# Kernel tuning notes

Measured on AMD Instinct MI355X. Metric: run time of the kernel, lower is better.

## Reference

```python
import jax, jax.numpy as jnp
import numpy as np
import math

B, S, H = 2, 2048, 2048
NH, NKV, HD = 16, 4, 128


def _rope_tables(seq_len, head_dim):
    # Standard RoPE: freqs over half dim, duplicated to full head_dim.
    inv_freq = 1.0 / (10000.0 ** (np.arange(0, head_dim, 2, dtype=np.float32) / head_dim))
    t = np.arange(seq_len, dtype=np.float32)
    freqs = np.outer(t, inv_freq)  # [S, HD/2]
    emb = np.concatenate([freqs, freqs], axis=-1)  # [S, HD]
    return jnp.asarray(np.cos(emb)), jnp.asarray(np.sin(emb))


def setup_inputs() -> dict:
    key = jax.random.key(0)
    k1, k2, k3, k4 = jax.random.split(key, 4)
    cos, sin = _rope_tables(S, HD)
    return {
        "x": jax.random.normal(k1, (B, S, H), dtype=jnp.float32),
        "cos": cos,
        "sin": sin,
        "Wq": jax.random.normal(k2, (H, NH * HD), dtype=jnp.float32) * (1.0 / math.sqrt(H)),
        "Wkv": jax.random.normal(k3, (H, 2 * NKV * HD), dtype=jnp.float32) * (1.0 / math.sqrt(H)),
        "Wo": jax.random.normal(k4, (NH * HD, H), dtype=jnp.float32) * (1.0 / math.sqrt(NH * HD)),
    }


def _rotate_half(x):
    x1, x2 = jnp.split(x, 2, axis=-1)
    return jnp.concatenate([-x2, x1], axis=-1)


def _apply_rotary(x, cos, sin):
    # x: [B, S, nheads, HD]; cos/sin: [S, HD]
    c = cos[None, :, None, :]
    s = sin[None, :, None, :]
    return x * c + _rotate_half(x) * s


def reference(x, cos, sin, Wq, Wkv, Wo):
    b, s, _ = x.shape
    q = (x @ Wq).reshape(b, s, NH, HD)
    kv = x @ Wkv
    k, v = jnp.split(kv, [NKV * HD], axis=-1)
    k = k.reshape(b, s, NKV, HD)
    v = v.reshape(b, s, NKV, HD)
    q = _apply_rotary(q, cos, sin)
    k = _apply_rotary(k, cos, sin)
    # to [B, heads, S, HD]
    q = jnp.transpose(q, (0, 2, 1, 3))
    k = jnp.transpose(k, (0, 2, 1, 3))
    v = jnp.transpose(v, (0, 2, 1, 3))
    # GQA: repeat K/V heads
    rep = NH // NKV
    k = jnp.repeat(k, rep, axis=1)
    v = jnp.repeat(v, rep, axis=1)
    scale = jnp.asarray(1.0 / math.sqrt(HD), dtype=x.dtype)
    scores = jnp.einsum('bhqd,bhkd->bhqk', q * scale, k)  # [B, NH, S, S]
    causal = jnp.tril(jnp.ones((s, s), dtype=jnp.bool_))
    scores = jnp.where(causal, scores, jnp.asarray(-jnp.inf, scores.dtype))
    attn = jax.nn.softmax(scores, axis=-1)
    out = jnp.einsum('bhqk,bhkd->bhqd', attn, v)
    out = jnp.transpose(out, (0, 2, 1, 3)).reshape(b, s, NH * HD)
    return out @ Wo
```

## Files before the change

kernel.cpp:

```cpp
#include <hip/hip_runtime.h>
#include <math.h>

#define NB 2
#define SEQ 2048
#define HDIM 2048
#define NHD 16
#define NKVH 4
#define HEADD 128
#define MROWS (NB*SEQ)
#define NQCOLS (NHD*HEADD)
#define QKVCOLS 3072

typedef unsigned short ushortT;
typedef __attribute__((ext_vector_type(8))) short short8;
typedef __attribute__((ext_vector_type(4))) float floatx4;
typedef __attribute__((ext_vector_type(4))) unsigned short ushort4v;

__device__ __forceinline__ ushortT f2bf(float f) {
  union { float f; unsigned int u; } v; v.f = f;
  unsigned int r = v.u + 0x7FFFu + ((v.u >> 16) & 1u);
  return (ushortT)(r >> 16);
}
__device__ __forceinline__ float bf2f(ushortT u) {
  union { unsigned int u; float f; } v; v.u = ((unsigned int)u) << 16;
  return v.f;
}

__device__ __forceinline__ unsigned int cvt_pk_bf16(float lo, float hi) {
  unsigned int r;
  asm("v_cvt_pk_bf16_f32 %0, %1, %2" : "=v"(r) : "v"(lo), "v"(hi));
  return r;
}

__device__ __forceinline__ void gload16(const ushortT* g, ushortT* l) {
  __builtin_amdgcn_global_load_lds(
      (const __attribute__((address_space(1))) void*)g,
      (__attribute__((address_space(3))) void*)l, 16, 0, 0);
}

__global__ __launch_bounds__(256) void cast_bf16_kernel(
    const float* __restrict__ in, ushortT* __restrict__ out, int n4) {
  int i = blockIdx.x * 256 + threadIdx.x;
  if (i >= n4) return;
  float4 v = ((const float4*)in)[i];
  ushort4v o;
  o.x = f2bf(v.x); o.y = f2bf(v.y); o.z = f2bf(v.z); o.w = f2bf(v.w);
  ((ushort4v*)out)[i] = o;
}

__global__ __launch_bounds__(256) void transpose_cast_kernel(
    const float* __restrict__ in, ushortT* __restrict__ out, int R, int C) {
  __shared__ ushortT tile[32][33];
  int c0 = blockIdx.x * 32, r0 = blockIdx.y * 32;
  int tx = threadIdx.x & 31, ty = threadIdx.x >> 5;
#pragma unroll
  for (int i = 0; i < 4; ++i)
    tile[ty + i*8][tx] = f2bf(in[(size_t)(r0 + ty + i*8) * C + c0 + tx]);
  __syncthreads();
#pragma unroll
  for (int i = 0; i < 4; ++i)
    out[(size_t)(c0 + ty + i*8) * R + r0 + tx] = tile[tx][ty + i*8];
}

__global__ __launch_bounds__(256) void gemm_bt_kernel(
    const ushortT* __restrict__ A, const ushortT* __restrict__ Bt,
    void* __restrict__ C, int M, int N, int K, int c_fp32) {
  __shared__ __align__(16) ushortT lA[128 * 64];
  __shared__ __align__(16) ushortT lB[128 * 64];
  const int m0 = blockIdx.y * 128;
  const int n0 = blockIdx.x * 128;
  const int tid = threadIdx.x;
  const int wave = tid >> 6, lane = tid & 63;
  const int g = lane >> 4, l15 = lane & 15;
  const int wm = (wave >> 1) * 64, wn = (wave & 1) * 64;
  const int sw = l15 & 7;

  floatx4 acc[4][4] = {};

  for (int kt = 0; kt < K; kt += 64) {
    __syncthreads();
#pragma unroll
    for (int i = 0; i < 4; ++i) {
      int s = i * 256 + tid;
      int r = s >> 3, j = s & 7;
      int col8 = j ^ (r & 7);
      gload16(A  + (size_t)(m0 + r) * K + kt + col8 * 8, lA + s * 8);
      gload16(Bt + (size_t)(n0 + r) * K + kt + col8 * 8, lB + s * 8);
    }
    __syncthreads();
#pragma unroll
    for (int ks = 0; ks < 2; ++ks) {
      short8 af[4], bfv[4];
#pragma unroll
      for (int t = 0; t < 4; ++t) {
        af[t]  = *(const short8*)(lA + (wm + t * 16 + l15) * 64 + ((ks * 4 + g) ^ sw) * 8);
        bfv[t] = *(const short8*)(lB + (wn + t * 16 + l15) * 64 + ((ks * 4 + g) ^ sw) * 8);
      }
#pragma unroll
      for (int mt = 0; mt < 4; ++mt)
#pragma unroll
        for (int nt = 0; nt < 4; ++nt)
          acc[mt][nt] = __builtin_amdgcn_mfma_f32_16x16x32_bf16(
              af[mt], bfv[nt], acc[mt][nt], 0, 0, 0);
    }
  }

#pragma unroll
  for (int mt = 0; mt < 4; ++mt)
#pragma unroll
    for (int nt = 0; nt < 4; ++nt)
#pragma unroll
      for (int r = 0; r < 4; ++r) {
        int row = m0 + wm + mt * 16 + g * 4 + r;
        int col = n0 + wn + nt * 16 + l15;
        float v = acc[mt][nt][r];
        if (c_fp32) ((float*)C)[(size_t)row * N + col] = v;
        else ((ushortT*)C)[(size_t)row * N + col] = f2bf(v);
      }
}

__global__ __launch_bounds__(256) void rope_q_kernel(
    const ushortT* __restrict__ QKVtmp, const float* __restrict__ cosT,
    const float* __restrict__ sinT, ushortT* __restrict__ Qr) {
  int idx = blockIdx.x * 256 + threadIdx.x;
  int d = idx & 63;
  int t = idx >> 6;
  int h = t & (NHD - 1);
  int bs = t >> 4;
  int s = bs & (SEQ - 1);
  int b = bs >> 11;
  float c = cosT[s * HEADD + d], sn = sinT[s * HEADD + d];
  float q1 = bf2f(QKVtmp[(size_t)bs * QKVCOLS + h * HEADD + d]);
  float q2 = bf2f(QKVtmp[(size_t)bs * QKVCOLS + h * HEADD + d + 64]);
  size_t o = ((size_t)(b * NHD + h) * SEQ + s) * HEADD + d;
  Qr[o]      = f2bf(q1 * c - q2 * sn);
  Qr[o + 64] = f2bf(q2 * c + q1 * sn);
}

__global__ __launch_bounds__(256) void rope_k_kernel(
    const ushortT* __restrict__ QKVtmp, const float* __restrict__ cosT,
    const float* __restrict__ sinT, ushortT* __restrict__ Kr) {
  int idx = blockIdx.x * 256 + threadIdx.x;
  int d = idx & 63;
  int t = idx >> 6;
  int kvh = t & (NKVH - 1);
  int bs = t >> 2;
  int s = bs & (SEQ - 1);
  int b = bs >> 11;
  float c = cosT[s * HEADD + d], sn = sinT[s * HEADD + d];
  float k1 = bf2f(QKVtmp[(size_t)bs * QKVCOLS + 2048 + kvh * HEADD + d]);
  float k2 = bf2f(QKVtmp[(size_t)bs * QKVCOLS + 2048 + kvh * HEADD + d + 64]);
  size_t o = ((size_t)(b * NKVH + kvh) * SEQ + s) * HEADD + d;
  Kr[o]      = f2bf(k1 * c - k2 * sn);
  Kr[o + 64] = f2bf(k2 * c + k1 * sn);
}

__global__ __launch_bounds__(256) void v_relayout_kernel(
    const ushortT* __restrict__ QKVtmp, ushortT* __restrict__ Vt) {
  __shared__ ushortT tile[32][33];
  int bk = blockIdx.z;
  int b = bk >> 2, kvh = bk & 3;
  int s0 = blockIdx.x * 32, d0 = blockIdx.y * 32;
  int tx = threadIdx.x & 31, ty = threadIdx.x >> 5;
#pragma unroll
  for (int i = 0; i < 4; ++i) {
    int s = s0 + ty + i * 8;
    tile[ty + i * 8][tx] =
        QKVtmp[(size_t)(b * SEQ + s) * QKVCOLS + 2560 + kvh * HEADD + d0 + tx];
  }
  __syncthreads();
#pragma unroll
  for (int i = 0; i < 4; ++i) {
    int d = d0 + ty + i * 8;
    Vt[((size_t)bk * HEADD + d) * SEQ + s0 + tx] = tile[tx][ty + i * 8];
  }
}

__global__ __launch_bounds__(256) void attn_kernel(
    const ushortT* __restrict__ Q,
    const ushortT* __restrict__ Kg,
    const ushortT* __restrict__ Vg,
    ushortT* __restrict__ Oa) {
  __shared__ __align__(16) ushortT lK[64 * 128];
  __shared__ __align__(16) ushortT lV[128 * 64];
  __shared__ __align__(16) ushortT lP[4 * 16 * 64];

  const int tid = threadIdx.x;
  const int w = tid >> 6, lane = tid & 63;
  const int g = lane >> 4, l15 = lane & 15;
  const int sw = l15 & 7;
  const int bh = blockIdx.x;
  const int b = bh >> 4, h = bh & 15;
  const int kvh = h >> 2;
  const int qi = 31 - (int)blockIdx.y;
  const int q0 = qi << 6;
  const int qw = q0 + w * 16;

  const float SC = 0.08838834764831845f * 1.4426950408889634f;
  const float THR = 8.0f / SC;

  short8 qf[4];
  {
    const ushortT* qp =
        Q + (((size_t)(b * NHD + h)) * SEQ + qw + l15) * HEADD + g * 8;
#pragma unroll
    for (int ks = 0; ks < 4; ++ks) qf[ks] = *(const short8*)(qp + ks * 32);
  }

  floatx4 o[8] = {};
  float m_s = -INFINITY;
  float l_s = 0.f;

  const ushortT* kbase = Kg + ((size_t)(b * NKVH + kvh)) * SEQ * HEADD;
  const ushortT* vbase = Vg + ((size_t)(b * NKVH + kvh)) * HEADD * SEQ;
  ushortT* pw = lP + w * 16 * 64;

  const int nkt = qi + 1;
  for (int kt = 0; kt < nkt; ++kt) {
    __syncthreads();
#pragma unroll
    for (int ii = 0; ii < 4; ++ii) {
      int s = ii * 256 + tid;
      int r = s >> 4, j = (s & 15) ^ (r & 7);
      gload16(kbase + (size_t)(kt * 64 + r) * HEADD + j * 8, lK + s * 8);
    }
#pragma unroll
    for (int ii = 0; ii < 4; ++ii) {
      int s = ii * 256 + tid;
      int r = s >> 3, j = (s & 7) ^ (r & 7);
      gload16(vbase + (size_t)r * SEQ + kt * 64 + j * 8, lV + s * 8);
    }
    __syncthreads();

    const int rel = qw - kt * 64;

    floatx4 sc[4] = {};
    __builtin_amdgcn_s_setprio(1);
#pragma unroll
    for (int nt = 0; nt < 4; ++nt) {
      if (nt * 16 > rel + 15) continue;
#pragma unroll
      for (int ks = 0; ks < 4; ++ks) {
        short8 kf = *(const short8*)(lK + (nt * 16 + l15) * 128 + ((ks * 4 + g) ^ sw) * 8);
        sc[nt] = __builtin_amdgcn_mfma_f32_16x16x32_bf16(kf, qf[ks], sc[nt], 0, 0, 0);
      }
    }
    __builtin_amdgcn_s_setprio(0);

    const bool needmask = (kt * 64 + 63) > qw;
    float ps[4][4];
    float mx = -INFINITY;
#pragma unroll
    for (int nt = 0; nt < 4; ++nt)
#pragma unroll
      for (int r = 0; r < 4; ++r) {
        float v = sc[nt][r];
        if (needmask) {
          int kg = kt * 64 + nt * 16 + g * 4 + r;
          if (kg > qw + l15) v = -INFINITY;
        }
        ps[nt][r] = v;
        mx = fmaxf(mx, v);
      }
    mx = fmaxf(mx, __shfl_xor(mx, 16));
    mx = fmaxf(mx, __shfl_xor(mx, 32));

    float mn;
    if (__all(mx <= m_s + THR)) {
      mn = m_s;
    } else {
      mn = fmaxf(m_s, mx);
      float alpha = __builtin_amdgcn_exp2f((m_s - mn) * SC);
      l_s *= alpha;
#pragma unroll
      for (int dt = 0; dt < 8; ++dt)
#pragma unroll
        for (int r = 0; r < 4; ++r) o[dt][r] *= alpha;
      m_s = mn;
    }
    const float mnSC = mn * SC;

    float rs = 0.f;
#pragma unroll
    for (int nt = 0; nt < 4; ++nt) {
      float e[4];
#pragma unroll
      for (int r = 0; r < 4; ++r) {
        e[r] = __builtin_amdgcn_exp2f(__builtin_fmaf(ps[nt][r], SC, -mnSC));
        rs += e[r];
      }
      uint2 pk;
      pk.x = cvt_pk_bf16(e[0], e[1]);
      pk.y = cvt_pk_bf16(e[2], e[3]);
      *(uint2*)(pw + l15 * 64 + (((nt * 2 + (g >> 1)) ^ sw) * 8 + (g & 1) * 4)) = pk;
    }
    rs += __shfl_xor(rs, 16);
    rs += __shfl_xor(rs, 32);
    l_s += rs;

    __builtin_amdgcn_s_setprio(1);
#pragma unroll
    for (int ks = 0; ks < 2; ++ks) {
      if (kt * 64 + ks * 32 > qw + 15) continue;
      short8 bp = *(const short8*)(pw + l15 * 64 + ((ks * 4 + g) ^ sw) * 8);
#pragma unroll
      for (int dt = 0; dt < 8; ++dt) {
        short8 vf = *(const short8*)(lV + (dt * 16 + l15) * 64 + ((ks * 4 + g) ^ sw) * 8);
        o[dt] = __builtin_amdgcn_mfma_f32_16x16x32_bf16(vf, bp, o[dt], 0, 0, 0);
      }
    }
    __builtin_amdgcn_s_setprio(0);
  }

  {
    float inv = 1.f / l_s;
    int qg = qw + l15;
#pragma unroll
    for (int dt = 0; dt < 8; ++dt) {
      uint2 ov;
      ov.x = cvt_pk_bf16(o[dt][0] * inv, o[dt][1] * inv);
      ov.y = cvt_pk_bf16(o[dt][2] * inv, o[dt][3] * inv);
      *(uint2*)(Oa + (size_t)(b * SEQ + qg) * NQCOLS + h * HEADD + dt * 16 + g * 4) = ov;
    }
  }
}

extern "C" void kernel_launch(void* const* d_in, const int* in_sizes, int n_in,
                              void* d_out, int out_size, void* d_ws, size_t ws_size,
                              hipStream_t stream) {
  const float* x    = (const float*)d_in[0];
  const float* cosT = (const float*)d_in[1];
  const float* sinT = (const float*)d_in[2];
  const float* Wq   = (const float*)d_in[3];
  const float* Wkv  = (const float*)d_in[4];
  const float* Wo   = (const float*)d_in[5];

  char* ws = (char*)d_ws;
  ushortT* x_bf   = (ushortT*)(ws + 0);
  ushortT* Wqkvt  = (ushortT*)(ws + 16777216);
  ushortT* Wot    = (ushortT*)(ws + 29360128);
  ushortT* QKVtmp = (ushortT*)(ws + 37748736);
  ushortT* Qr     = (ushortT*)(ws + 62914560);
  ushortT* Kr     = (ushortT*)(ws + 79691776);
  ushortT* Vt     = (ushortT*)(ws + 83886080);
  ushortT* Oattn  = QKVtmp;

  cast_bf16_kernel<<<8192, 256, 0, stream>>>(x, x_bf, (MROWS * HDIM) / 4);
  transpose_cast_kernel<<<dim3(64, 64), 256, 0, stream>>>(Wq, Wqkvt, HDIM, NQCOLS);
  transpose_cast_kernel<<<dim3(32, 64), 256, 0, stream>>>(Wkv, Wqkvt + 2048 * 2048, HDIM, 1024);
  transpose_cast_kernel<<<dim3(64, 64), 256, 0, stream>>>(Wo, Wot, NQCOLS, HDIM);

  gemm_bt_kernel<<<dim3(24, 32), 256, 0, stream>>>(x_bf, Wqkvt, QKVtmp, MROWS, QKVCOLS, HDIM, 0);

  rope_q_kernel<<<16384, 256, 0, stream>>>(QKVtmp, cosT, sinT, Qr);
  rope_k_kernel<<<4096, 256, 0, stream>>>(QKVtmp, cosT, sinT, Kr);
  v_relayout_kernel<<<dim3(64, 4, 8), 256, 0, stream>>>(QKVtmp, Vt);

  attn_kernel<<<dim3(32, 32), 256, 0, stream>>>(Qr, Kr, Vt, Oattn);

  gemm_bt_kernel<<<dim3(16, 32), 256, 0, stream>>>(Oattn, Wot, d_out, MROWS, HDIM, NQCOLS, 1);
}
```

Baseline: 339.2 us.

## Pair causal query tiles per block and double-buffer K/V loads

Each attention block now processes two query tiles, one long and one short in causal length (qi=31-y and qi=y). This evens out the work per block and halves the grid. K/V tiles are double-buffered in LDS, so the next tile's global-to-LDS load is issued before the current tile's compute, with one barrier per iteration. The cost is twice the K/V LDS footprint, which may reduce occupancy, and more registers for the two Q fragment sets.

```diff
diff --git a/kernel.cpp b/kernel.cpp
--- a/kernel.cpp
+++ b/kernel.cpp
@@ -181,8 +181,8 @@
     const ushortT* __restrict__ Kg,
     const ushortT* __restrict__ Vg,
     ushortT* __restrict__ Oa) {
-  __shared__ __align__(16) ushortT lK[64 * 128];
-  __shared__ __align__(16) ushortT lV[128 * 64];
+  __shared__ __align__(16) ushortT lK[2][64 * 128];
+  __shared__ __align__(16) ushortT lV[2][128 * 64];
   __shared__ __align__(16) ushortT lP[4 * 16 * 64];
 
   const int tid = threadIdx.x;
@@ -192,57 +192,63 @@
   const int bh = blockIdx.x;
   const int b = bh >> 4, h = bh & 15;
   const int kvh = h >> 2;
-  const int qi = 31 - (int)blockIdx.y;
-  const int q0 = qi << 6;
-  const int qw = q0 + w * 16;
+  const int yi = blockIdx.y;
+  const int qiA = 31 - yi;
+  const int qiB = yi;
+  const int nA = qiA + 1, nB = qiB + 1;
 
   const float SC = 0.08838834764831845f * 1.4426950408889634f;
   const float THR = 8.0f / SC;
 
-  short8 qf[4];
+  const ushortT* kbase = Kg + ((size_t)(b * NKVH + kvh)) * SEQ * HEADD;
+  const ushortT* vbase = Vg + ((size_t)(b * NKVH + kvh)) * HEADD * SEQ;
+  ushortT* pw = lP + w * 16 * 64;
+
+  const int qwA = (qiA << 6) + w * 16;
+  const int qwB = (qiB << 6) + w * 16;
+
+  short8 qfA[4], qfB[4];
   {
-    const ushortT* qp =
-        Q + (((size_t)(b * NHD + h)) * SEQ + qw + l15) * HEADD + g * 8;
-#pragma unroll
-    for (int ks = 0; ks < 4; ++ks) qf[ks] = *(const short8*)(qp + ks * 32);
+    const ushortT* qpA = Q + (((size_t)(b * NHD + h)) * SEQ + qwA + l15) * HEADD + g * 8;
+    const ushortT* qpB = Q + (((size_t)(b * NHD + h)) * SEQ + qwB + l15) * HEADD + g * 8;
+#pragma unroll
+    for (int ks = 0; ks < 4; ++ks) {
+      qfA[ks] = *(const short8*)(qpA + ks * 32);
+      qfB[ks] = *(const short8*)(qpB + ks * 32);
+    }
   }
 
   floatx4 o[8] = {};
   float m_s = -INFINITY;
   float l_s = 0.f;
 
-  const ushortT* kbase = Kg + ((size_t)(b * NKVH + kvh)) * SEQ * HEADD;
-  const ushortT* vbase = Vg + ((size_t)(b * NKVH + kvh)) * HEADD * SEQ;
-  ushortT* pw = lP + w * 16 * 64;
-
-  const int nkt = qi + 1;
-  for (int kt = 0; kt < nkt; ++kt) {
-    __syncthreads();
+  auto stage = [&](int kt, int buf) {
 #pragma unroll
     for (int ii = 0; ii < 4; ++ii) {
       int s = ii * 256 + tid;
       int r = s >> 4, j = (s & 15) ^ (r & 7);
-      gload16(kbase + (size_t)(kt * 64 + r) * HEADD + j * 8, lK + s * 8);
+      gload16(kbase + (size_t)(kt * 64 + r) * HEADD + j * 8, lK[buf] + s * 8);
     }
 #pragma unroll
     for (int ii = 0; ii < 4; ++ii) {
       int s = ii * 256 + tid;
       int r = s >> 3, j = (s & 7) ^ (r & 7);
-      gload16(vbase + (size_t)r * SEQ + kt * 64 + j * 8, lV + s * 8);
-    }
-    __syncthreads();
-
+      gload16(vbase + (size_t)r * SEQ + kt * 64 + j * 8, lV[buf] + s * 8);
+    }
+  };
+
+  auto compute = [&](const short8 (&qf)[4], int qw, int kt, int cur) {
     const int rel = qw - kt * 64;
 
-    floatx4 sc[4] = {};
+    floatx4 sc4[4] = {};
     __builtin_amdgcn_s_setprio(1);
 #pragma unroll
     for (int nt = 0; nt < 4; ++nt) {
       if (nt * 16 > rel + 15) continue;
 #pragma unroll
       for (int ks = 0; ks < 4; ++ks) {
-        short8 kf = *(const short8*)(lK + (nt * 16 + l15) * 128 + ((ks * 4 + g) ^ sw) * 8);
-        sc[nt] = __builtin_amdgcn_mfma_f32_16x16x32_bf16(kf, qf[ks], sc[nt], 0, 0, 0);
+        short8 kf = *(const short8*)(lK[cur] + (nt * 16 + l15) * 128 + ((ks * 4 + g) ^ sw) * 8);
+        sc4[nt] = __builtin_amdgcn_mfma_f32_16x16x32_bf16(kf, qf[ks], sc4[nt], 0, 0, 0);
       }
     }
     __builtin_amdgcn_s_setprio(0);
@@ -254,7 +260,7 @@
     for (int nt = 0; nt < 4; ++nt)
 #pragma unroll
       for (int r = 0; r < 4; ++r) {
-        float v = sc[nt][r];
+        float v = sc4[nt][r];
         if (needmask) {
           int kg = kt * 64 + nt * 16 + g * 4 + r;
           if (kg > qw + l15) v = -INFINITY;
@@ -305,14 +311,14 @@
       short8 bp = *(const short8*)(pw + l15 * 64 + ((ks * 4 + g) ^ sw) * 8);
 #pragma unroll
       for (int dt = 0; dt < 8; ++dt) {
-        short8 vf = *(const short8*)(lV + (dt * 16 + l15) * 64 + ((ks * 4 + g) ^ sw) * 8);
+        short8 vf = *(const short8*)(lV[cur] + (dt * 16 + l15) * 64 + ((ks * 4 + g) ^ sw) * 8);
         o[dt] = __builtin_amdgcn_mfma_f32_16x16x32_bf16(vf, bp, o[dt], 0, 0, 0);
       }
     }
     __builtin_amdgcn_s_setprio(0);
-  }
-
-  {
+  };
+
+  auto epilogue = [&](int qw) {
     float inv = 1.f / l_s;
     int qg = qw + l15;
 #pragma unroll
@@ -322,7 +328,33 @@
       ov.y = cvt_pk_bf16(o[dt][2] * inv, o[dt][3] * inv);
       *(uint2*)(Oa + (size_t)(b * SEQ + qg) * NQCOLS + h * HEADD + dt * 16 + g * 4) = ov;
     }
-  }
+  };
+
+  stage(0, 0);
+  asm volatile("s_waitcnt vmcnt(0)" ::: "memory");
+  __builtin_amdgcn_s_barrier();
+
+  for (int kt = 0; kt < nA; ++kt) {
+    const int cur = kt & 1;
+    if (kt + 1 < nA) stage(kt + 1, cur ^ 1);
+    else             stage(0, cur ^ 1);
+    compute(qfA, qwA, kt, cur);
+    asm volatile("s_waitcnt vmcnt(0)" ::: "memory");
+    __builtin_amdgcn_s_barrier();
+  }
+  epilogue(qwA);
+#pragma unroll
+  for (int dt = 0; dt < 8; ++dt) o[dt] = floatx4{0.f, 0.f, 0.f, 0.f};
+  m_s = -INFINITY; l_s = 0.f;
+
+  for (int kt = 0; kt < nB; ++kt) {
+    const int cur = (nA + kt) & 1;
+    if (kt + 1 < nB) stage(kt + 1, cur ^ 1);
+    compute(qfB, qwB, kt, cur);
+    asm volatile("s_waitcnt vmcnt(0)" ::: "memory");
+    __builtin_amdgcn_s_barrier();
+  }
+  epilogue(qwB);
 }
 
 extern "C" void kernel_launch(void* const* d_in, const int* in_sizes, int n_in,
@@ -356,7 +388,7 @@
   rope_k_kernel<<<4096, 256, 0, stream>>>(QKVtmp, cosT, sinT, Kr);
   v_relayout_kernel<<<dim3(64, 4, 8), 256, 0, stream>>>(QKVtmp, Vt);
 
-  attn_kernel<<<dim3(32, 32), 256, 0, stream>>>(Qr, Kr, Vt, Oattn);
+  attn_kernel<<<dim3(32, 16), 256, 0, stream>>>(Qr, Kr, Vt, Oattn);
 
   gemm_bt_kernel<<<dim3(16, 32), 256, 0, stream>>>(Oattn, Wot, d_out, MROWS, HDIM, NQCOLS, 1);
 }
```

Result: no change. 339.5 us (+0.1%).
